# Kernel tuning notes

Measured on AMD Instinct MI355X. Metric: run time of the kernel, lower is better.

## Reference

```python
import jax, jax.numpy as jnp
import numpy as np

D_MODEL = 1024
N_HEAD = 16
D_FF = 4096
B, S = 2, 2048


def _layernorm(x, g, b, eps=1e-5):
    mu = jnp.mean(x, axis=-1, keepdims=True)
    var = jnp.var(x, axis=-1, keepdims=True)
    return (x - mu) * jax.lax.rsqrt(var + eps) * g + b


def setup_inputs() -> dict:
    key = jax.random.key(0)
    ks = jax.random.split(key, 12)
    s = 0.02
    return {
        "x": jax.random.normal(ks[0], (B, S, D_MODEL), dtype=jnp.float32),
        "src_mask": jnp.zeros((B, 1, 1, S), dtype=jnp.float32),
        "w_q": jax.random.normal(ks[1], (D_MODEL, D_MODEL), dtype=jnp.float32) * s,
        "b_q": jnp.zeros((D_MODEL,), dtype=jnp.float32),
        "w_k": jax.random.normal(ks[2], (D_MODEL, D_MODEL), dtype=jnp.float32) * s,
        "b_k": jnp.zeros((D_MODEL,), dtype=jnp.float32),
        "w_v": jax.random.normal(ks[3], (D_MODEL, D_MODEL), dtype=jnp.float32) * s,
        "b_v": jnp.zeros((D_MODEL,), dtype=jnp.float32),
        "w_o": jax.random.normal(ks[4], (D_MODEL, D_MODEL), dtype=jnp.float32) * s,
        "b_o": jnp.zeros((D_MODEL,), dtype=jnp.float32),
        "w_ff1": jax.random.normal(ks[5], (D_MODEL, D_FF), dtype=jnp.float32) * s,
        "b_ff1": jnp.zeros((D_FF,), dtype=jnp.float32),
        "w_ff2": jax.random.normal(ks[6], (D_FF, D_MODEL), dtype=jnp.float32) * s,
        "b_ff2": jnp.zeros((D_MODEL,), dtype=jnp.float32),
        "ln1_g": jnp.ones((D_MODEL,), dtype=jnp.float32),
        "ln1_b": jnp.zeros((D_MODEL,), dtype=jnp.float32),
        "ln2_g": jnp.ones((D_MODEL,), dtype=jnp.float32),
        "ln2_b": jnp.zeros((D_MODEL,), dtype=jnp.float32),
    }


def reference(x, src_mask, w_q, b_q, w_k, b_k, w_v, b_v, w_o, b_o,
              w_ff1, b_ff1, w_ff2, b_ff2, ln1_g, ln1_b, ln2_g, ln2_b):
    b, s, d = x.shape
    dh = d // N_HEAD

    def split(t):  # [b,s,d] -> [b,h,s,dh]
        return t.reshape(b, s, N_HEAD, dh).transpose(0, 2, 1, 3)

    q = split(x @ w_q + b_q)
    k = split(x @ w_k + b_k)
    v = split(x @ w_v + b_v)

    # naive full-score attention, as in the source module
    score = jnp.einsum('bhqd,bhkd->bhqk', q, k) / jnp.sqrt(jnp.float32(dh))
    score = score + src_mask
    attn = jax.nn.softmax(score, axis=-1)
    out = jnp.einsum('bhqk,bhkd->bhqd', attn, v)
    out = out.transpose(0, 2, 1, 3).reshape(b, s, d)
    out = out @ w_o + b_o

    x = _layernorm(x + out, ln1_g, ln1_b)

    ff = jax.nn.relu(x @ w_ff1 + b_ff1) @ w_ff2 + b_ff2
    x = _layernorm(x + ff, ln2_g, ln2_b)
    return x
```

## Files before the change

### kernel.cpp

```cpp
#include <hip/hip_runtime.h>
#include <cstdint>
#include <cstddef>

#define BATCH 2
#define SEQ 2048
#define DMODEL 1024
#define NHEAD 16
#define DFF 4096
#define MTOT (BATCH * SEQ)

typedef __bf16 bf16x8 __attribute__((ext_vector_type(8)));
typedef __bf16 bf16x4 __attribute__((ext_vector_type(4)));
typedef short s16x4 __attribute__((ext_vector_type(4)));
typedef float f32x4 __attribute__((ext_vector_type(4)));

#define S_BARRIER() __builtin_amdgcn_s_barrier()
#define SCHED_FENCE() __builtin_amdgcn_sched_barrier(0)
#define VMCNT8() asm volatile("s_waitcnt vmcnt(8)" ::: "memory")
#define VMCNT4() asm volatile("s_waitcnt vmcnt(4)" ::: "memory")
#define VMCNT0() asm volatile("s_waitcnt vmcnt(0)" ::: "memory")

__device__ __forceinline__ void gload_lds16(const void* g, void* l) {
  __builtin_amdgcn_global_load_lds(
      (__attribute__((address_space(1))) void*)(uintptr_t)g,
      (__attribute__((address_space(3))) void*)(uint32_t)(uintptr_t)l,
      16, 0, 0);
}

__global__ __launch_bounds__(256) void k_transpose_to_bf16(
    const float* __restrict__ w, __bf16* __restrict__ wt, int K, int N) {
  __shared__ float t[32][33];
  const int n0 = blockIdx.x * 32, k0 = blockIdx.y * 32;
  const int tx = threadIdx.x & 31, ty = threadIdx.x >> 5;
#pragma unroll
  for (int i = ty; i < 32; i += 8) t[i][tx] = w[(size_t)(k0 + i) * N + n0 + tx];
  __syncthreads();
#pragma unroll
  for (int i = ty; i < 32; i += 8)
    wt[(size_t)(n0 + i) * K + k0 + tx] = (__bf16)t[tx][i];
}

__global__ __launch_bounds__(256) void k_cvt_bf16(
    const float* __restrict__ in, __bf16* __restrict__ out, int n) {
  const int i = (blockIdx.x * 256 + threadIdx.x) * 4;
  if (i >= n) return;
  const float4 v = *(const float4*)(in + i);
  bf16x4 r;
  r[0] = (__bf16)v.x; r[1] = (__bf16)v.y; r[2] = (__bf16)v.z; r[3] = (__bf16)v.w;
  *(bf16x4*)(out + i) = r;
}

__global__ void k_concat3(const float* __restrict__ a, const float* __restrict__ b,
                          const float* __restrict__ c, float* __restrict__ o) {
  const int i = blockIdx.x * 256 + threadIdx.x;
  if (i >= 3072) return;
  o[i] = (i < 1024) ? a[i] : (i < 2048) ? b[i - 1024] : c[i - 2048];
}

__global__ void k_scale_mask(const float* __restrict__ in, float* __restrict__ o, int n) {
  const int i = blockIdx.x * 256 + threadIdx.x;
  if (i < n) o[i] = in[i] * 1.44269504f;
}

__global__ __launch_bounds__(256) void k_transpose_v(
    const __bf16* __restrict__ qkvb, __bf16* __restrict__ vT) {
  __shared__ __bf16 t[32][33];
  const int s0 = blockIdx.x * 32, c0 = blockIdx.y * 32, b = blockIdx.z;
  const int tx = threadIdx.x & 31, ty = threadIdx.x >> 5;
#pragma unroll
  for (int i = ty; i < 32; i += 8)
    t[i][tx] = qkvb[(size_t)(b * SEQ + s0 + i) * 3072 + 2048 + c0 + tx];
  __syncthreads();
#pragma unroll
  for (int i = ty; i < 32; i += 8)
    vT[((size_t)b * 1024 + c0 + i) * SEQ + s0 + tx] = t[tx][i];
}

template <bool RELU, typename OutT>
__global__ __launch_bounds__(512) void k_gemm256(
    const __bf16* __restrict__ A, const __bf16* __restrict__ BT,
    const float* __restrict__ bias, OutT* __restrict__ C,
    int M, int N, int K) {
  __shared__ __align__(16) __bf16 sA[4 * 8192];
  __shared__ __align__(16) __bf16 sB[4 * 8192];
  const int tid = threadIdx.x, lane = tid & 63, wv = tid >> 6;
  const int wm = wv >> 2, wn = wv & 3;
  const int lrow = lane & 15, hi = lane >> 4;
  const int nwg = gridDim.x * gridDim.y;
  const int flat = blockIdx.y * gridDim.x + blockIdx.x;
  const int cpx = nwg >> 3;
  const int swzb = (flat & 7) * cpx + (flat >> 3);
  const int m0 = (swzb / gridDim.x) * 256;
  const int n0 = (swzb % gridDim.x) * 256;
  const int NT = K >> 6;

  const int lsub = lane >> 2;
  const int gg = (lane & 3) ^ ((lane >> 3) & 3);
  const int gr = hi ^ ((lrow >> 1) & 3);

  f32x4 acc[8][4];
#pragma unroll
  for (int r = 0; r < 8; ++r)
#pragma unroll
    for (int c = 0; c < 4; ++c) acc[r][c] = f32x4{0.f, 0.f, 0.f, 0.f};

  auto stage = [&](int p) {
    const int tile = p >> 1;
    const int slot = (((tile & 1) * 2) + (p & 1)) * 8192;
    const int kcol = tile * 64 + (p & 1) * 32 + gg * 8;
#pragma unroll
    for (int i = 0; i < 2; ++i) {
      const int c = wv * 2 + i;
      gload_lds16(A + (size_t)(m0 + c * 16 + lsub) * K + kcol, &sA[slot + c * 512]);
      gload_lds16(BT + (size_t)(n0 + c * 16 + lsub) * K + kcol, &sB[slot + c * 512]);
    }
  };

  auto compute = [&](int p) {
    const int slot = ((((p >> 1) & 1) * 2) + (p & 1)) * 8192;
    bf16x8 af[8], bfv[4];
#pragma unroll
    for (int r = 0; r < 8; ++r)
      af[r] = *(const bf16x8*)&sA[slot + (wm * 128 + r * 16 + lrow) * 32 + gr * 8];
#pragma unroll
    for (int c = 0; c < 4; ++c)
      bfv[c] = *(const bf16x8*)&sB[slot + (wn * 64 + c * 16 + lrow) * 32 + gr * 8];
    __builtin_amdgcn_s_setprio(1);
#pragma unroll
    for (int r = 0; r < 8; ++r)
#pragma unroll
      for (int c = 0; c < 4; ++c)
        acc[r][c] = __builtin_amdgcn_mfma_f32_16x16x32_bf16(af[r], bfv[c],
                                                            acc[r][c], 0, 0, 0);
    __builtin_amdgcn_s_setprio(0);
  };

  stage(0); stage(1); stage(2);
  int p = 0;
  for (; p < 2 * NT - 3; ++p) {
    VMCNT8(); S_BARRIER(); SCHED_FENCE();
    stage(p + 3);
    compute(p);
  }
  VMCNT8(); S_BARRIER(); SCHED_FENCE(); compute(p); ++p;
  VMCNT4(); S_BARRIER(); SCHED_FENCE(); compute(p); ++p;
  VMCNT0(); S_BARRIER(); SCHED_FENCE(); compute(p);

#pragma unroll
  for (int r = 0; r < 8; ++r) {
    const int row = m0 + wm * 128 + r * 16 + hi * 4;
#pragma unroll
    for (int c = 0; c < 4; ++c) {
      const int col = n0 + wn * 64 + c * 16 + lrow;
      const float bb = bias[col];
#pragma unroll
      for (int j = 0; j < 4; ++j) {
        float v = acc[r][c][j] + bb;
        if (RELU) v = fmaxf(v, 0.f);
        C[(size_t)(row + j) * N + col] = (OutT)v;
      }
    }
  }
}

template <int MF, bool RELU, typename OutT>
__global__ __launch_bounds__(256) void k_gemm(
    const __bf16* __restrict__ A, const __bf16* __restrict__ BT,
    const float* __restrict__ bias, OutT* __restrict__ C, int M, int N, int K) {
  __shared__ __bf16 sA[MF * 32 * 64];
  __shared__ __bf16 sB[128 * 64];
  const int tid = threadIdx.x, lane = tid & 63, wv = tid >> 6;
  const int wm = wv >> 1, wn = wv & 1;
  const int lrow = lane & 15, hi = lane >> 4;
  const int nwg = gridDim.x * gridDim.y;
  const int flat = blockIdx.y * gridDim.x + blockIdx.x;
  const int cpx = nwg >> 3;
  const int swzb = (flat & 7) * cpx + (flat >> 3);
  const int m0 = (swzb / gridDim.x) * (MF * 32);
  const int n0 = (swzb % gridDim.x) * 128;
  const int srow = lane >> 3;
  const int scolE = ((lane & 7) ^ srow) * 8;
  const int swz = (lrow & 7) << 4;

  f32x4 acc[MF][4];
#pragma unroll
  for (int r = 0; r < MF; ++r)
#pragma unroll
    for (int c = 0; c < 4; ++c) acc[r][c] = f32x4{0.f, 0.f, 0.f, 0.f};

  for (int k0 = 0; k0 < K; k0 += 64) {
    __syncthreads();
#pragma unroll
    for (int rb = wv; rb < MF * 4; rb += 4) {
      const int row = rb * 8 + srow;
      gload_lds16(A + (size_t)(m0 + row) * K + k0 + scolE, &sA[rb * 512]);
    }
#pragma unroll
    for (int rb = wv; rb < 16; rb += 4) {
      const int row = rb * 8 + srow;
      gload_lds16(BT + (size_t)(n0 + row) * K + k0 + scolE, &sB[rb * 512]);
    }
    __syncthreads();
#pragma unroll
    for (int kc = 0; kc < 2; ++kc) {
      bf16x8 af[MF], bfr[4];
#pragma unroll
      for (int r = 0; r < MF; ++r) {
        const int row = wm * (MF * 16) + r * 16 + lrow;
        af[r] = *(const bf16x8*)((const char*)sA + row * 128 + ((kc * 64 + hi * 16) ^ swz));
      }
#pragma unroll
      for (int c = 0; c < 4; ++c) {
        const int row = wn * 64 + c * 16 + lrow;
        bfr[c] = *(const bf16x8*)((const char*)sB + row * 128 + ((kc * 64 + hi * 16) ^ swz));
      }
#pragma unroll
      for (int r = 0; r < MF; ++r)
#pragma unroll
        for (int c = 0; c < 4; ++c)
          acc[r][c] = __builtin_amdgcn_mfma_f32_16x16x32_bf16(af[r], bfr[c],
                                                              acc[r][c], 0, 0, 0);
    }
  }

#pragma unroll
  for (int r = 0; r < MF; ++r) {
    const int row = m0 + wm * (MF * 16) + r * 16 + hi * 4;
#pragma unroll
    for (int c = 0; c < 4; ++c) {
      const int col = n0 + wn * 64 + c * 16 + lrow;
      const float bb = bias[col];
#pragma unroll
      for (int j = 0; j < 4; ++j) {
        float v = acc[r][c][j] + bb;
        if (RELU) v = fmaxf(v, 0.f);
        C[(size_t)(row + j) * N + col] = (OutT)v;
      }
    }
  }
}

__global__ __launch_bounds__(256) void k_attn(
    const __bf16* __restrict__ qkv, const __bf16* __restrict__ vT,
    const float* __restrict__ mask2, __bf16* __restrict__ out) {
  const int qb = blockIdx.x, h = blockIdx.y, b = blockIdx.z;
  const int tid = threadIdx.x, lane = tid & 63, wv = tid >> 6;
  const int lrow = lane & 15, hi = lane >> 4;

  __shared__ __bf16 sK[2][64 * 64];
  __shared__ __bf16 sV[2][64 * 64];

  const size_t base = (size_t)b * SEQ * 3072;
  const __bf16* Qb = qkv + base + h * 64;
  const __bf16* Kb = qkv + base + 1024 + h * 64;
  const __bf16* vTb = vT + ((size_t)b * 1024 + h * 64) * SEQ;
  const float* maskb = mask2 + (size_t)b * SEQ;

  const int q0 = qb * 64 + wv * 16;
  const bf16x8 qf0 = *(const bf16x8*)&Qb[(size_t)(q0 + lrow) * 3072 + hi * 8];
  const bf16x8 qf1 = *(const bf16x8*)&Qb[(size_t)(q0 + lrow) * 3072 + 32 + hi * 8];

  float m_r = -3e38f, l_r = 0.f;
  f32x4 o[4];
#pragma unroll
  for (int d = 0; d < 4; ++d) o[d] = f32x4{0.f, 0.f, 0.f, 0.f};

  const int srow = lane >> 3;
  const int scolE = ((lane & 7) ^ srow) * 8;
  const int swz = (lrow & 7) << 4;

  auto stage = [&](int t) {
    const int k0s = t * 64;
    __bf16* dK = sK[t & 1];
    __bf16* dV = sV[t & 1];
#pragma unroll
    for (int r = 0; r < 2; ++r) {
      const int rb = r * 4 + wv;
      const int row = rb * 8 + srow;
      gload_lds16(Kb + (size_t)(k0s + row) * 3072 + scolE, &dK[rb * 512]);
      gload_lds16(vTb + (size_t)row * SEQ + k0s + scolE, &dV[rb * 512]);
    }
  };

  stage(0);
  const int NT = SEQ / 64;
  for (int t = 0; t < NT; ++t) {
    __syncthreads();
    if (t + 1 < NT) stage(t + 1);
    const __bf16* cK = sK[t & 1];
    const __bf16* cV = sV[t & 1];
    const int k0 = t * 64;

    f32x4 st[4];
#pragma unroll
    for (int t4 = 0; t4 < 4; ++t4) {
      const char* rp = (const char*)cK + (t4 * 16 + lrow) * 128;
      const bf16x8 ka = *(const bf16x8*)(rp + ((hi * 16) ^ swz));
      const bf16x8 kb = *(const bf16x8*)(rp + ((64 + hi * 16) ^ swz));
      f32x4 a = f32x4{0.f, 0.f, 0.f, 0.f};
      a = __builtin_amdgcn_mfma_f32_16x16x32_bf16(ka, qf0, a, 0, 0, 0);
      a = __builtin_amdgcn_mfma_f32_16x16x32_bf16(kb, qf1, a, 0, 0, 0);
      st[t4] = a;
    }

    float pm = -3e38f;
#pragma unroll
    for (int t4 = 0; t4 < 4; ++t4) {
      const f32x4 mk = *(const f32x4*)&maskb[k0 + t4 * 16 + hi * 4];
#pragma unroll
      for (int j = 0; j < 4; ++j) {
        st[t4][j] = st[t4][j] * 0.18033688f + mk[j];
        pm = fmaxf(pm, st[t4][j]);
      }
    }
    pm = fmaxf(pm, __shfl_xor(pm, 16));
    pm = fmaxf(pm, __shfl_xor(pm, 32));

    if (__any(pm > m_r + 11.5f)) {
      const float mn = fmaxf(m_r, pm);
      const float so = __builtin_amdgcn_exp2f(m_r - mn);
      m_r = mn;
      l_r *= so;
      float so_o[4];
#pragma unroll
      for (int jj = 0; jj < 4; ++jj) so_o[jj] = __shfl(so, hi * 4 + jj);
#pragma unroll
      for (int d = 0; d < 4; ++d)
#pragma unroll
        for (int jj = 0; jj < 4; ++jj) o[d][jj] *= so_o[jj];
    }

    float rs = 0.f;
#pragma unroll
    for (int t4 = 0; t4 < 4; ++t4)
#pragma unroll
      for (int j = 0; j < 4; ++j) {
        st[t4][j] = __builtin_amdgcn_exp2f(st[t4][j] - m_r);
        rs += st[t4][j];
      }
    rs += __shfl_xor(rs, 16);
    rs += __shfl_xor(rs, 32);
    l_r += rs;

    s16x4 pa[4];
#pragma unroll
    for (int t4 = 0; t4 < 4; ++t4)
#pragma unroll
      for (int j = 0; j < 4; ++j) {
        const __bf16 pb = (__bf16)st[t4][j];
        pa[t4][j] = __builtin_bit_cast(short, pb);
      }

#pragma unroll
    for (int d = 0; d < 4; ++d) {
      const char* rp = (const char*)cV + (d * 16 + lrow) * 128;
#pragma unroll
      for (int t4 = 0; t4 < 4; ++t4) {
        const s16x4 vb = *(const s16x4*)(rp + ((t4 * 32 + hi * 8) ^ swz));
        o[d] = __builtin_amdgcn_mfma_f32_16x16x16bf16_1k(pa[t4], vb, o[d], 0, 0, 0);
      }
    }
  }

  __syncthreads();
  float linv[4];
#pragma unroll
  for (int jj = 0; jj < 4; ++jj) linv[jj] = 1.0f / __shfl(l_r, hi * 4 + jj);
#pragma unroll
  for (int d = 0; d < 4; ++d)
#pragma unroll
    for (int jj = 0; jj < 4; ++jj)
      out[((size_t)b * SEQ + q0 + hi * 4 + jj) * DMODEL + h * 64 + d * 16 + lrow] =
          (__bf16)(o[d][jj] * linv[jj]);
}

__global__ __launch_bounds__(256) void k_add_ln(
    const float* __restrict__ x, const float* __restrict__ y,
    const float* __restrict__ g, const float* __restrict__ be,
    float* __restrict__ of, __bf16* __restrict__ ob) {
  const int row = blockIdx.x, tid = threadIdx.x;
  const float4 a = ((const float4*)(x + (size_t)row * 1024))[tid];
  const float4 b = ((const float4*)(y + (size_t)row * 1024))[tid];
  const float v0 = a.x + b.x, v1 = a.y + b.y, v2 = a.z + b.z, v3 = a.w + b.w;
  float s = v0 + v1 + v2 + v3;
  float s2 = v0 * v0 + v1 * v1 + v2 * v2 + v3 * v3;
#pragma unroll
  for (int off = 32; off > 0; off >>= 1) {
    s += __shfl_xor(s, off);
    s2 += __shfl_xor(s2, off);
  }
  __shared__ float red[2][4];
  const int wv = tid >> 6, lane = tid & 63;
  if (lane == 0) { red[0][wv] = s; red[1][wv] = s2; }
  __syncthreads();
  s = red[0][0] + red[0][1] + red[0][2] + red[0][3];
  s2 = red[1][0] + red[1][1] + red[1][2] + red[1][3];
  const float mean = s * (1.0f / 1024.0f);
  const float var = s2 * (1.0f / 1024.0f) - mean * mean;
  const float rstd = rsqrtf(var + 1e-5f);
  const float4 gg = ((const float4*)g)[tid];
  const float4 bt = ((const float4*)be)[tid];
  float4 r;
  r.x = (v0 - mean) * rstd * gg.x + bt.x;
  r.y = (v1 - mean) * rstd * gg.y + bt.y;
  r.z = (v2 - mean) * rstd * gg.z + bt.z;
  r.w = (v3 - mean) * rstd * gg.w + bt.w;
  ((float4*)(of + (size_t)row * 1024))[tid] = r;
  if (ob) {
    bf16x4 rb;
    rb[0] = (__bf16)r.x; rb[1] = (__bf16)r.y; rb[2] = (__bf16)r.z; rb[3] = (__bf16)r.w;
    *(bf16x4*)(ob + (size_t)row * 1024 + tid * 4) = rb;
  }
}

extern "C" void kernel_launch(void* const* d_in, const int* in_sizes, int n_in,
                              void* d_out, int out_size, void* d_ws, size_t ws_size,
                              hipStream_t stream) {
  const float* x = (const float*)d_in[0];
  const float* src_mask = (const float*)d_in[1];
  const float* w_q = (const float*)d_in[2];
  const float* b_q = (const float*)d_in[3];
  const float* w_k = (const float*)d_in[4];
  const float* b_k = (const float*)d_in[5];
  const float* w_v = (const float*)d_in[6];
  const float* b_v = (const float*)d_in[7];
  const float* w_o = (const float*)d_in[8];
  const float* b_o = (const float*)d_in[9];
  const float* w_ff1 = (const float*)d_in[10];
  const float* b_ff1 = (const float*)d_in[11];
  const float* w_ff2 = (const float*)d_in[12];
  const float* b_ff2 = (const float*)d_in[13];
  const float* ln1_g = (const float*)d_in[14];
  const float* ln1_b = (const float*)d_in[15];
  const float* ln2_g = (const float*)d_in[16];
  const float* ln2_b = (const float*)d_in[17];

  char* ws = (char*)d_ws;
  constexpr size_t O_WQKVT = 0;
  constexpr size_t O_WOT = O_WQKVT + 3072ull * 1024 * 2;
  constexpr size_t O_WFF1T = O_WOT + 1024ull * 1024 * 2;
  constexpr size_t O_WFF2T = O_WFF1T + 4096ull * 1024 * 2;
  constexpr size_t O_BQKV = O_WFF2T + 4096ull * 1024 * 2;
  constexpr size_t O_XBF = O_BQKV + 3072ull * 4;
  constexpr size_t O_QKV = O_XBF + 4096ull * 1024 * 2;
  constexpr size_t O_ATTN = O_QKV + 4096ull * 3072 * 2;
  constexpr size_t O_PROJ = O_ATTN + 4096ull * 1024 * 2;
  constexpr size_t O_H1F = O_PROJ + 4096ull * 1024 * 4;
  constexpr size_t O_H1B = O_H1F + 4096ull * 1024 * 4;
  constexpr size_t O_MASK2 = O_H1B + 4096ull * 1024 * 2;
  constexpr size_t O_VT = O_PROJ;
  constexpr size_t O_FF = O_QKV;
  constexpr size_t O_FF2 = O_PROJ;

  __bf16* wqkvT = (__bf16*)(ws + O_WQKVT);
  __bf16* woT = (__bf16*)(ws + O_WOT);
  __bf16* wff1T = (__bf16*)(ws + O_WFF1T);
  __bf16* wff2T = (__bf16*)(ws + O_WFF2T);
  float* bqkv = (float*)(ws + O_BQKV);
  __bf16* xbf = (__bf16*)(ws + O_XBF);
  __bf16* qkvb = (__bf16*)(ws + O_QKV);
  __bf16* attnb = (__bf16*)(ws + O_ATTN);
  float* proj = (float*)(ws + O_PROJ);
  float* h1f = (float*)(ws + O_H1F);
  __bf16* h1b = (__bf16*)(ws + O_H1B);
  float* mask2 = (float*)(ws + O_MASK2);
  __bf16* vT = (__bf16*)(ws + O_VT);
  __bf16* ffb = (__bf16*)(ws + O_FF);
  float* ff2 = (float*)(ws + O_FF2);

  k_transpose_to_bf16<<<dim3(32, 32), 256, 0, stream>>>(w_q, wqkvT, 1024, 1024);
  k_transpose_to_bf16<<<dim3(32, 32), 256, 0, stream>>>(w_k, wqkvT + 1024 * 1024, 1024, 1024);
  k_transpose_to_bf16<<<dim3(32, 32), 256, 0, stream>>>(w_v, wqkvT + 2 * 1024 * 1024, 1024, 1024);
  k_transpose_to_bf16<<<dim3(32, 32), 256, 0, stream>>>(w_o, woT, 1024, 1024);
  k_transpose_to_bf16<<<dim3(128, 32), 256, 0, stream>>>(w_ff1, wff1T, 1024, 4096);
  k_transpose_to_bf16<<<dim3(32, 128), 256, 0, stream>>>(w_ff2, wff2T, 4096, 1024);
  k_concat3<<<12, 256, 0, stream>>>(b_q, b_k, b_v, bqkv);
  k_scale_mask<<<16, 256, 0, stream>>>(src_mask, mask2, BATCH * SEQ);
  k_cvt_bf16<<<4096, 256, 0, stream>>>(x, xbf, MTOT * DMODEL);

  k_gemm256<false, __bf16><<<dim3(12, 16), 512, 0, stream>>>(xbf, wqkvT, bqkv, qkvb,
                                                             MTOT, 3072, 1024);
  k_transpose_v<<<dim3(64, 32, 2), 256, 0, stream>>>(qkvb, vT);
  k_attn<<<dim3(SEQ / 64, NHEAD, BATCH), 256, 0, stream>>>(qkvb, vT, mask2, attnb);
  k_gemm<2, false, float><<<dim3(8, 64), 256, 0, stream>>>(attnb, woT, b_o, proj,
                                                           MTOT, 1024, 1024);
  k_add_ln<<<4096, 256, 0, stream>>>(x, proj, ln1_g, ln1_b, h1f, h1b);
  k_gemm256<true, __bf16><<<dim3(16, 16), 512, 0, stream>>>(h1b, wff1T, b_ff1, ffb,
                                                            MTOT, DFF, 1024);
  k_gemm<2, false, float><<<dim3(8, 64), 256, 0, stream>>>(ffb, wff2T, b_ff2, ff2,
                                                           MTOT, 1024, DFF);
  k_add_ln<<<4096, 256, 0, stream>>>(h1f, ff2, ln2_g, ln2_b, (float*)d_out, nullptr);
}
```

Baseline: 274.8 us.

## Split attention over key halves and merge partial softmax results

After: 286.2 us. 4.1% more time.

```diff
diff --git a/kernel.cpp b/kernel.cpp
--- a/kernel.cpp
+++ b/kernel.cpp
@@ -242,13 +242,16 @@
 
 __global__ __launch_bounds__(256) void k_attn(
     const __bf16* __restrict__ qkv, const __bf16* __restrict__ vT,
-    const float* __restrict__ mask2, __bf16* __restrict__ out) {
-  const int qb = blockIdx.x, h = blockIdx.y, b = blockIdx.z;
+    const float* __restrict__ mask2, float* __restrict__ po,
+    float* __restrict__ pl, float* __restrict__ pmv) {
+  const int qb = blockIdx.x, h = blockIdx.y, bz = blockIdx.z;
+  const int b = bz & 1, split = bz >> 1;
+  const int koff = split * (SEQ / 2);
   const int tid = threadIdx.x, lane = tid & 63, wv = tid >> 6;
   const int lrow = lane & 15, hi = lane >> 4;
 
-  __shared__ __bf16 sK[2][64 * 64];
-  __shared__ __bf16 sV[2][64 * 64];
+  __shared__ __bf16 sK[64 * 64];
+  __shared__ __bf16 sV[64 * 64];
 
   const size_t base = (size_t)b * SEQ * 3072;
   const __bf16* Qb = qkv + base + h * 64;
@@ -269,32 +272,21 @@
   const int scolE = ((lane & 7) ^ srow) * 8;
   const int swz = (lrow & 7) << 4;
 
-  auto stage = [&](int t) {
-    const int k0s = t * 64;
-    __bf16* dK = sK[t & 1];
-    __bf16* dV = sV[t & 1];
+  for (int k0 = 0; k0 < SEQ / 2; k0 += 64) {
+    __syncthreads();
 #pragma unroll
     for (int r = 0; r < 2; ++r) {
       const int rb = r * 4 + wv;
       const int row = rb * 8 + srow;
-      gload_lds16(Kb + (size_t)(k0s + row) * 3072 + scolE, &dK[rb * 512]);
-      gload_lds16(vTb + (size_t)row * SEQ + k0s + scolE, &dV[rb * 512]);
-    }
-  };
-
-  stage(0);
-  const int NT = SEQ / 64;
-  for (int t = 0; t < NT; ++t) {
+      gload_lds16(Kb + (size_t)(koff + k0 + row) * 3072 + scolE, &sK[rb * 512]);
+      gload_lds16(vTb + (size_t)row * SEQ + koff + k0 + scolE, &sV[rb * 512]);
+    }
     __syncthreads();
-    if (t + 1 < NT) stage(t + 1);
-    const __bf16* cK = sK[t & 1];
-    const __bf16* cV = sV[t & 1];
-    const int k0 = t * 64;
 
     f32x4 st[4];
 #pragma unroll
     for (int t4 = 0; t4 < 4; ++t4) {
-      const char* rp = (const char*)cK + (t4 * 16 + lrow) * 128;
+      const char* rp = (const char*)sK + (t4 * 16 + lrow) * 128;
       const bf16x8 ka = *(const bf16x8*)(rp + ((hi * 16) ^ swz));
       const bf16x8 kb = *(const bf16x8*)(rp + ((64 + hi * 16) ^ swz));
       f32x4 a = f32x4{0.f, 0.f, 0.f, 0.f};
@@ -306,7 +298,7 @@
     float pm = -3e38f;
 #pragma unroll
     for (int t4 = 0; t4 < 4; ++t4) {
-      const f32x4 mk = *(const f32x4*)&maskb[k0 + t4 * 16 + hi * 4];
+      const f32x4 mk = *(const f32x4*)&maskb[koff + k0 + t4 * 16 + hi * 4];
 #pragma unroll
       for (int j = 0; j < 4; ++j) {
         st[t4][j] = st[t4][j] * 0.18033688f + mk[j];
@@ -353,7 +345,7 @@
 
 #pragma unroll
     for (int d = 0; d < 4; ++d) {
-      const char* rp = (const char*)cV + (d * 16 + lrow) * 128;
+      const char* rp = (const char*)sV + (d * 16 + lrow) * 128;
 #pragma unroll
       for (int t4 = 0; t4 < 4; ++t4) {
         const s16x4 vb = *(const s16x4*)(rp + ((t4 * 32 + hi * 8) ^ swz));
@@ -362,16 +354,42 @@
     }
   }
 
-  __syncthreads();
-  float linv[4];
-#pragma unroll
-  for (int jj = 0; jj < 4; ++jj) linv[jj] = 1.0f / __shfl(l_r, hi * 4 + jj);
+  const size_t porow = (size_t)(split * BATCH + b) * SEQ;
 #pragma unroll
   for (int d = 0; d < 4; ++d)
 #pragma unroll
     for (int jj = 0; jj < 4; ++jj)
-      out[((size_t)b * SEQ + q0 + hi * 4 + jj) * DMODEL + h * 64 + d * 16 + lrow] =
-          (__bf16)(o[d][jj] * linv[jj]);
+      po[(porow + q0 + hi * 4 + jj) * 1024 + h * 64 + d * 16 + lrow] = o[d][jj];
+  if (lane < 16) {
+    const size_t li = ((size_t)(split * BATCH + b) * NHEAD + h) * SEQ + q0 + lane;
+    pl[li] = l_r;
+    pmv[li] = m_r;
+  }
+}
+
+__global__ __launch_bounds__(256) void k_merge(
+    const float* __restrict__ po, const float* __restrict__ pl,
+    const float* __restrict__ pmv, __bf16* __restrict__ out) {
+  const int s = blockIdx.x, b = blockIdx.y;
+  const int col = threadIdx.x * 4;
+  const int h = col >> 6;
+  const size_t r1 = ((size_t)b * SEQ + s) * 1024;
+  const size_t r2 = ((size_t)(BATCH + b) * SEQ + s) * 1024;
+  const float4 o1 = *(const float4*)(po + r1 + col);
+  const float4 o2 = *(const float4*)(po + r2 + col);
+  const size_t li1 = ((size_t)b * NHEAD + h) * SEQ + s;
+  const size_t li2 = ((size_t)(BATCH + b) * NHEAD + h) * SEQ + s;
+  const float m1 = pmv[li1], m2 = pmv[li2];
+  const float m = fmaxf(m1, m2);
+  const float w1 = __builtin_amdgcn_exp2f(m1 - m);
+  const float w2 = __builtin_amdgcn_exp2f(m2 - m);
+  const float inv = 1.0f / (pl[li1] * w1 + pl[li2] * w2);
+  bf16x4 r;
+  r[0] = (__bf16)((o1.x * w1 + o2.x * w2) * inv);
+  r[1] = (__bf16)((o1.y * w1 + o2.y * w2) * inv);
+  r[2] = (__bf16)((o1.z * w1 + o2.z * w2) * inv);
+  r[3] = (__bf16)((o1.w * w1 + o2.w * w2) * inv);
+  *(bf16x4*)(out + r1 + col) = r;
 }
 
 __global__ __launch_bounds__(256) void k_add_ln(
@@ -448,7 +466,10 @@
   constexpr size_t O_H1F = O_PROJ + 4096ull * 1024 * 4;
   constexpr size_t O_H1B = O_H1F + 4096ull * 1024 * 4;
   constexpr size_t O_MASK2 = O_H1B + 4096ull * 1024 * 2;
-  constexpr size_t O_VT = O_PROJ;
+  constexpr size_t O_VT = O_H1B;
+  constexpr size_t O_PO = O_PROJ;
+  constexpr size_t O_PL = O_XBF;
+  constexpr size_t O_PM = O_XBF + (512ull << 10);
   constexpr size_t O_FF = O_QKV;
   constexpr size_t O_FF2 = O_PROJ;
 
@@ -465,6 +486,9 @@
   __bf16* h1b = (__bf16*)(ws + O_H1B);
   float* mask2 = (float*)(ws + O_MASK2);
   __bf16* vT = (__bf16*)(ws + O_VT);
+  float* po = (float*)(ws + O_PO);
+  float* pl = (float*)(ws + O_PL);
+  float* pm = (float*)(ws + O_PM);
   __bf16* ffb = (__bf16*)(ws + O_FF);
   float* ff2 = (float*)(ws + O_FF2);
 
@@ -481,7 +505,9 @@
   k_gemm256<false, __bf16><<<dim3(12, 16), 512, 0, stream>>>(xbf, wqkvT, bqkv, qkvb,
                                                              MTOT, 3072, 1024);
   k_transpose_v<<<dim3(64, 32, 2), 256, 0, stream>>>(qkvb, vT);
-  k_attn<<<dim3(SEQ / 64, NHEAD, BATCH), 256, 0, stream>>>(qkvb, vT, mask2, attnb);
+  k_attn<<<dim3(SEQ / 64, NHEAD, BATCH * 2), 256, 0, stream>>>(qkvb, vT, mask2,
+                                                               po, pl, pm);
+  k_merge<<<dim3(SEQ, BATCH), 256, 0, stream>>>(po, pl, pm, attnb);
   k_gemm<2, false, float><<<dim3(8, 64), 256, 0, stream>>>(attnb, woT, b_o, proj,
                                                            MTOT, 1024, 1024);
   k_add_ln<<<4096, 256, 0, stream>>>(x, proj, ln1_g, ln1_b, h1f, h1b);
```
